# Kernel optimization log

Hardware: AMD Instinct MI355X
Metric: run time of the kernel (lower is better)

Reference implementation:

```python
import jax, jax.numpy as jnp
import numpy as np

D_MODEL = 1024
NUM_HEADS = 16
D_K = D_MODEL // NUM_HEADS
ROPE_THETA = 10000.0


def setup_inputs() -> dict:
    key = jax.random.key(0)
    kx, kq, kk, kv, ko = jax.random.split(key, 5)
    B, S = 4, 2048
    std = (2.0 / (D_MODEL + D_MODEL)) ** 0.5
    def w(k):
        return jax.random.truncated_normal(k, -3.0, 3.0, (D_MODEL, D_MODEL), jnp.float32) * std
    return {
        "x": jax.random.normal(kx, (B, S, D_MODEL), jnp.float32),
        "Wq": w(kq), "Wk": w(kk), "Wv": w(kv), "Wo": w(ko),
    }


def _apply_rope(t):
    # t: [B, H, S, d_k]
    S, dk = t.shape[-2], t.shape[-1]
    inv_freq = 1.0 / (ROPE_THETA ** (jnp.arange(0, dk, 2) / dk))  # [dk/2]
    angles = jnp.outer(jnp.arange(S), inv_freq)                    # [S, dk/2]
    cos = jnp.repeat(jnp.cos(angles), 2, axis=-1).astype(t.dtype)  # [S, dk]
    sin = jnp.repeat(jnp.sin(angles), 2, axis=-1).astype(t.dtype)
    t_even = t[..., 0::2]
    t_odd = t[..., 1::2]
    t_rot = jnp.stack([-t_odd, t_even], axis=-1).reshape(t.shape)
    return t * cos + t_rot * sin


def reference(x, Wq, Wk, Wv, Wo):
    B, S, D = x.shape
    H, dk = NUM_HEADS, D_K
    q = jnp.einsum("bsi,io->bso", x, Wq).reshape(B, S, H, dk).swapaxes(1, 2)
    k = jnp.einsum("bsi,io->bso", x, Wk).reshape(B, S, H, dk).swapaxes(1, 2)
    v = jnp.einsum("bsi,io->bso", x, Wv).reshape(B, S, H, dk).swapaxes(1, 2)
    q = _apply_rope(q)
    k = _apply_rope(k)
    scores = jnp.einsum("bhqd,bhkd->bhqk", q, k) / (dk ** 0.5)  # [B,H,S,S]
    causal = jnp.tril(jnp.ones((S, S), dtype=bool))
    scores = jnp.where(causal, scores, -jnp.inf)
    attn = jax.nn.softmax(scores, axis=-1)
    out = jnp.einsum("bhqk,bhkd->bhqd", attn, v)  # [B,H,S,dk]
    out = out.swapaxes(1, 2).reshape(B, S, D)
    return jnp.einsum("bsi,io->bso", out, Wo)
```

## Files before the change

kernel.cpp:

```cpp
#include <hip/hip_runtime.h>
#include <hip/hip_bf16.h>

#define SEQ   2048
#define NB    4
#define NH    16
#define DK    64
#define DM    1024
#define MROWS (NB * SEQ)

typedef __bf16 bf16_t;
typedef __bf16 bf16x8 __attribute__((ext_vector_type(8)));
typedef __bf16 bf16x4 __attribute__((ext_vector_type(4)));
typedef float  f32x4  __attribute__((ext_vector_type(4)));

#define MFMA16(a, b, c) __builtin_amdgcn_mfma_f32_16x16x32_bf16((a), (b), (c), 0, 0, 0)

__device__ __forceinline__ void gl2lds16(const bf16_t* g, bf16_t* l) {
    __builtin_amdgcn_global_load_lds(
        (const __attribute__((address_space(1))) unsigned int*)g,
        (__attribute__((address_space(3))) unsigned int*)l, 16, 0, 0);
}

__global__ __launch_bounds__(256) void cvt_kernel(
    const float* __restrict__ in, bf16_t* __restrict__ out, int n)
{
    int i = (blockIdx.x * 256 + threadIdx.x) * 4;
    if (i + 3 < n) {
        const float4 v = *(const float4*)(in + i);
        bf16x4 o;
        o[0] = (bf16_t)v.x; o[1] = (bf16_t)v.y;
        o[2] = (bf16_t)v.z; o[3] = (bf16_t)v.w;
        *(bf16x4*)(out + i) = o;
    }
}

__global__ __launch_bounds__(256) void wtr_kernel(
    const float* __restrict__ W, bf16_t* __restrict__ Wt)
{
    __shared__ float T[32][33];
    const int tk0 = (blockIdx.x >> 5) << 5;
    const int tn0 = (blockIdx.x & 31) << 5;
    const int r = threadIdx.x >> 5, c = threadIdx.x & 31;
#pragma unroll
    for (int i = 0; i < 4; ++i)
        T[r + i * 8][c] = W[(size_t)(tk0 + r + i * 8) * DM + tn0 + c];
    __syncthreads();
#pragma unroll
    for (int i = 0; i < 4; ++i)
        Wt[(size_t)(tn0 + r + i * 8) * DM + tk0 + c] = (bf16_t)T[c][r + i * 8];
}

__global__ void rope_table_kernel(float2* __restrict__ tab) {
    int idx = blockIdx.x * 256 + threadIdx.x;
    if (idx >= SEQ * 32) return;
    int s = idx >> 5, i = idx & 31;
    float freq = powf(10000.0f, -(float)i / 32.0f);
    float a = (float)s * freq;
    tab[idx] = make_float2(cosf(a), sinf(a));
}

#define SBAR()   asm volatile("s_barrier" ::: "memory")
#define VMC(N)   asm volatile("s_waitcnt vmcnt(" #N ")" ::: "memory")

template<bool TR>
__device__ __forceinline__ void kloop256(
    const bf16_t* __restrict__ Xp, const bf16_t* __restrict__ Wp,
    bf16_t* L, int tid, f32x4 (&acc)[8][4], int kt)
{
    const int lane = tid & 63;
    const int wave = tid >> 6;
    const int wm   = wave & 1;
    const int wn   = wave >> 1;
    const int lrow = lane & 15;
    const int lcol = (lane >> 4) << 3;

    bf16_t* const As = L;
    bf16_t* const Bs = L + 4 * 8192;

    auto stA = [&](int t, int half) {
        const bf16_t* g = Xp + (size_t)(half * 128 + wave * 16 + lrow) * DM + t * 64 + lcol;
        bf16_t* s = As + ((t & 1) * 2 + half) * 8192 + wave * 1024;
        gl2lds16(g,      s);
        gl2lds16(g + 32, s + 512);
    };
    auto stB = [&](int t, int half) {
        const bf16_t* g = Wp + (size_t)(half * 128 + wave * 16 + lrow) * DM + t * 64 + lcol;
        bf16_t* s = Bs + ((t & 1) * 2 + half) * 8192 + wave * 1024;
        gl2lds16(g,      s);
        gl2lds16(g + 32, s + 512);
    };

    const bf16_t* const Aw = As + wm * 8192;
    const bf16_t* const Bw = Bs + (wn >> 1) * 8192;
    const int bgrp = (wn & 1) * 4;

    stA(0, 0); stA(0, 1); stB(0, 0); stB(0, 1);
    stB(1, 0); stB(1, 1);
    VMC(4);
    SBAR();

    const int nit = kt >> 1;
    for (int it = 0; it < nit; ++it) {
        const int t = 2 * it;
        const bool lst = (t + 2 >= kt);

#pragma unroll
        for (int par = 0; par < 2; ++par) {
            bf16x8 bf[8];
#pragma unroll
            for (int q = 0; q < 4; ++q) {
                const bf16_t* ap = Aw + par * 16384;
                bf16x8 a00 = *(const bf16x8*)(ap + (q * 4 + 0) * 512 + lane * 8);
                bf16x8 a01 = *(const bf16x8*)(ap + (q * 4 + 1) * 512 + lane * 8);
                bf16x8 a10 = *(const bf16x8*)(ap + (q * 4 + 2) * 512 + lane * 8);
                bf16x8 a11 = *(const bf16x8*)(ap + (q * 4 + 3) * 512 + lane * 8);
                if (q == 0) {
                    const bf16_t* bp = Bw + par * 16384;
#pragma unroll
                    for (int nf = 0; nf < 4; ++nf) {
                        bf[nf * 2]     = *(const bf16x8*)(bp + ((bgrp + nf) * 2 + 0) * 512 + lane * 8);
                        bf[nf * 2 + 1] = *(const bf16x8*)(bp + ((bgrp + nf) * 2 + 1) * 512 + lane * 8);
                    }
                }
                if (par == 0) {
                    if (q == 0) { stA(t + 1, 0); stA(t + 1, 1); }
                    else if (q == 1) { if (!lst) stB(t + 2, 0); }
                    else if (q == 2) { if (!lst) stB(t + 2, 1); }
                } else {
                    if (q == 0)      { if (!lst) stA(t + 2, 0); }
                    else if (q == 1) { if (!lst) stA(t + 2, 1); }
                    else if (q == 2) { if (!lst) stB(t + 3, 0); }
                    else             { if (!lst) stB(t + 3, 1); }
                }
                SBAR();
                __builtin_amdgcn_s_setprio(1);
#pragma unroll
                for (int nf = 0; nf < 4; ++nf) {
                    if (TR) {
                        acc[q * 2 + 0][nf] = MFMA16(bf[nf * 2],     a00, acc[q * 2 + 0][nf]);
                        acc[q * 2 + 0][nf] = MFMA16(bf[nf * 2 + 1], a01, acc[q * 2 + 0][nf]);
                        acc[q * 2 + 1][nf] = MFMA16(bf[nf * 2],     a10, acc[q * 2 + 1][nf]);
                        acc[q * 2 + 1][nf] = MFMA16(bf[nf * 2 + 1], a11, acc[q * 2 + 1][nf]);
                    } else {
                        acc[q * 2 + 0][nf] = MFMA16(a00, bf[nf * 2],     acc[q * 2 + 0][nf]);
                        acc[q * 2 + 0][nf] = MFMA16(a01, bf[nf * 2 + 1], acc[q * 2 + 0][nf]);
                        acc[q * 2 + 1][nf] = MFMA16(a10, bf[nf * 2],     acc[q * 2 + 1][nf]);
                        acc[q * 2 + 1][nf] = MFMA16(a11, bf[nf * 2 + 1], acc[q * 2 + 1][nf]);
                    }
                }
                __builtin_amdgcn_s_setprio(0);
                if (q == 3) {
                    if (par == 0) { if (lst) { VMC(0); } else { VMC(4); } }
                    else          { if (!lst) { VMC(4); } }
                }
                SBAR();
            }
        }
    }
    VMC(0);
}

__global__ __launch_bounds__(512, 2) void gemm_qkv_kernel(
    const bf16_t* __restrict__ X, const bf16_t* __restrict__ Wt,
    bf16_t* __restrict__ Qt, bf16_t* __restrict__ Kt, bf16_t* __restrict__ Vtr,
    const float2* __restrict__ rope)
{
    __shared__ __align__(16) bf16_t L[8 * 8192];

    const int tid = threadIdx.x;
    const int xcd = blockIdx.x & 7;
    const int idx = blockIdx.x >> 3;
    const int mt  = xcd * 4 + idx / 12;
    const int nt  = idx % 12;
    const int m0 = mt << 8, n0 = nt << 8;
    const bool tr = (n0 >= 2 * DM);

    f32x4 acc[8][4] = {};
    if (tr) kloop256<true >(X + (size_t)m0 * DM, Wt + (size_t)n0 * DM, L, tid, acc, DM / 64);
    else    kloop256<false>(X + (size_t)m0 * DM, Wt + (size_t)n0 * DM, L, tid, acc, DM / 64);

    const int lane = tid & 63;
    const int wave = tid >> 6;
    const int wm   = wave & 1, wn = wave >> 1;
    const int l    = lane & 15;
    const int quad = lane >> 4;

#pragma unroll
    for (int mf = 0; mf < 8; ++mf)
#pragma unroll
        for (int nf = 0; nf < 4; ++nf)
#pragma unroll
            for (int r = 0; r < 4; ++r) {
                float v = acc[mf][nf][r];
                if (tr) {
                    const int n = n0 + wn * 64 + nf * 16 + quad * 4 + r;
                    const int m = m0 + wm * 128 + mf * 16 + l;
                    const int bi = m >> 11, s = m & (SEQ - 1);
                    const int col = n & (DM - 1);
                    const int h = col >> 6, d = col & (DK - 1);
                    Vtr[(((size_t)(bi * NH + h)) * DK + d) * SEQ + s] = (bf16_t)v;
                } else {
                    const int m  = m0 + wm * 128 + mf * 16 + quad * 4 + r;
                    const int nn = n0 + wn * 64 + nf * 16 + l;
                    const int bi = m >> 11, s = m & (SEQ - 1);
                    const int col = nn & (DM - 1);
                    const int h = col >> 6, d = col & (DK - 1);
                    float pv = __shfl_xor(v, 1);
                    float2 cs = rope[s * 32 + (d >> 1)];
                    float res = (d & 1) ? (v * cs.x + pv * cs.y)
                                        : (v * cs.x - pv * cs.y);
                    bf16_t* dst = (nn < DM) ? Qt : Kt;
                    if (nn < DM) res *= 0.125f;
                    dst[(((size_t)(bi * NH + h)) * SEQ + s) * DK + d] = (bf16_t)res;
                }
            }
}

__global__ __launch_bounds__(512, 2) void gemm_out_kernel(
    const bf16_t* __restrict__ X, const bf16_t* __restrict__ Wt,
    float* __restrict__ out)
{
    __shared__ __align__(16) bf16_t L[8 * 8192];

    const int tid = threadIdx.x;
    const int xcd = blockIdx.x & 7;
    const int idx = blockIdx.x >> 3;
    const int mt  = xcd * 4 + idx / 4;
    const int nt  = idx & 3;
    const int m0 = mt << 8, n0 = nt << 8;

    f32x4 acc[8][4] = {};
    kloop256<false>(X + (size_t)m0 * DM, Wt + (size_t)n0 * DM, L, tid, acc, DM / 64);

    const int lane = tid & 63;
    const int wave = tid >> 6;
    const int wm   = wave & 1, wn = wave >> 1;
    const int l    = lane & 15;
    const int quad = lane >> 4;

#pragma unroll
    for (int mf = 0; mf < 8; ++mf)
#pragma unroll
        for (int nf = 0; nf < 4; ++nf)
#pragma unroll
            for (int r = 0; r < 4; ++r) {
                const int m  = m0 + wm * 128 + mf * 16 + quad * 4 + r;
                const int nn = n0 + wn * 64 + nf * 16 + l;
                out[(size_t)m * DM + nn] = acc[mf][nf][r];
            }
}

#define KLD 72

__global__ __launch_bounds__(256) void attn_kernel(
    const bf16_t* __restrict__ Q, const bf16_t* __restrict__ K,
    const bf16_t* __restrict__ Vt, bf16_t* __restrict__ O)
{
    __shared__ __align__(16) bf16_t Kl[64 * KLD];
    __shared__ __align__(16) bf16_t Vl[64 * KLD];
    __shared__ __align__(16) bf16_t Pl[4][32 * KLD];

    const int bh   = blockIdx.x;
    const int qx   = blockIdx.y;
    const int tid  = threadIdx.x;
    const int wave = tid >> 6;
    const int lane = tid & 63;
    const int l    = lane & 15;
    const int quad = lane >> 4;
    const int srow = tid >> 3;
    const int sch  = (tid & 7) << 3;

    bf16_t* Pw = Pl[wave];
    const bf16_t* Qb = Q  + (size_t)bh * SEQ * DK;
    const bf16_t* Kb = K  + (size_t)bh * SEQ * DK;
    const bf16_t* Vb = Vt + (size_t)bh * DK * SEQ;
    const int b = bh >> 4, h = bh & 15;

    for (int ph = 0; ph < 2; ++ph) {
        const int qblk = ph ? (15 - qx) : qx;
        const int q0w  = qblk * 128 + wave * 32;
        const int nch  = 2 * (qblk + 1);

        bf16x8 qb[2][2];
#pragma unroll
        for (int u = 0; u < 2; ++u) {
            qb[u][0] = *(const bf16x8*)(Qb + (size_t)(q0w + u * 16 + l) * DK + quad * 8);
            qb[u][1] = *(const bf16x8*)(Qb + (size_t)(q0w + u * 16 + l) * DK + 32 + quad * 8);
        }

        float m_run[2] = {-3e38f, -3e38f};
        float l_run[2] = {0.f, 0.f};
        f32x4 o[4][2] = {};

        bf16x8 pk0 = *(const bf16x8*)(Kb + (size_t)srow * DK + sch);
        bf16x8 pk1 = *(const bf16x8*)(Kb + (size_t)(32 + srow) * DK + sch);
        bf16x8 pv0 = *(const bf16x8*)(Vb + (size_t)srow * SEQ + sch);
        bf16x8 pv1 = *(const bf16x8*)(Vb + (size_t)(32 + srow) * SEQ + sch);

        for (int i = 0; i < nch; ++i) {
            const int c = i * 64;
            __syncthreads();
            *(bf16x8*)(Kl + srow * KLD + sch)        = pk0;
            *(bf16x8*)(Kl + (32 + srow) * KLD + sch) = pk1;
            *(bf16x8*)(Vl + srow * KLD + sch)        = pv0;
            *(bf16x8*)(Vl + (32 + srow) * KLD + sch) = pv1;
            __syncthreads();
            if (i + 1 < nch) {
                const int cn = c + 64;
                pk0 = *(const bf16x8*)(Kb + (size_t)(cn + srow) * DK + sch);
                pk1 = *(const bf16x8*)(Kb + (size_t)(cn + 32 + srow) * DK + sch);
                pv0 = *(const bf16x8*)(Vb + (size_t)srow * SEQ + cn + sch);
                pv1 = *(const bf16x8*)(Vb + (size_t)(32 + srow) * SEQ + cn + sch);
            }
            if (c > q0w + 31) continue;

            f32x4 st[4][2] = {};
#pragma unroll
            for (int t = 0; t < 4; ++t) {
                const bf16x8 k0 = *(const bf16x8*)(Kl + (t * 16 + l) * KLD + quad * 8);
                const bf16x8 k1 = *(const bf16x8*)(Kl + (t * 16 + l) * KLD + 32 + quad * 8);
                st[t][0] = MFMA16(k0, qb[0][0], st[t][0]);
                st[t][0] = MFMA16(k1, qb[0][1], st[t][0]);
                st[t][1] = MFMA16(k0, qb[1][0], st[t][1]);
                st[t][1] = MFMA16(k1, qb[1][1], st[t][1]);
            }
            if (c + 63 > q0w) {
#pragma unroll
                for (int u = 0; u < 2; ++u) {
                    const int thr = q0w + u * 16 + l - c - quad * 4;
#pragma unroll
                    for (int t = 0; t < 4; ++t)
#pragma unroll
                        for (int r = 0; r < 4; ++r)
                            if (t * 16 + r > thr) st[t][u][r] = -3e38f;
                }
            }
#pragma unroll
            for (int u = 0; u < 2; ++u) {
                float cmax = -3e38f;
#pragma unroll
                for (int t = 0; t < 4; ++t)
#pragma unroll
                    for (int r = 0; r < 4; ++r)
                        cmax = fmaxf(cmax, st[t][u][r]);
                cmax = fmaxf(cmax, __shfl_xor(cmax, 16));
                cmax = fmaxf(cmax, __shfl_xor(cmax, 32));
                const float mnew  = fmaxf(m_run[u], cmax);
                const float alpha = __expf(m_run[u] - mnew);
                m_run[u] = mnew;
                float csum = 0.f;
#pragma unroll
                for (int t = 0; t < 4; ++t)
#pragma unroll
                    for (int r = 0; r < 4; ++r) {
                        st[t][u][r] = __expf(st[t][u][r] - mnew);
                        csum += st[t][u][r];
                    }
                csum += __shfl_xor(csum, 16);
                csum += __shfl_xor(csum, 32);
                l_run[u] = l_run[u] * alpha + csum;
#pragma unroll
                for (int n = 0; n < 4; ++n)
#pragma unroll
                    for (int r = 0; r < 4; ++r)
                        o[n][u][r] *= alpha;
#pragma unroll
                for (int t = 0; t < 4; ++t) {
                    bf16x4 pk;
                    pk[0] = (bf16_t)st[t][u][0]; pk[1] = (bf16_t)st[t][u][1];
                    pk[2] = (bf16_t)st[t][u][2]; pk[3] = (bf16_t)st[t][u][3];
                    *(bf16x4*)(Pw + (u * 16 + l) * KLD + t * 16 + quad * 4) = pk;
                }
            }
            const bf16x8 pb00 = *(const bf16x8*)(Pw + l * KLD + quad * 8);
            const bf16x8 pb01 = *(const bf16x8*)(Pw + l * KLD + 32 + quad * 8);
            const bf16x8 pb10 = *(const bf16x8*)(Pw + (16 + l) * KLD + quad * 8);
            const bf16x8 pb11 = *(const bf16x8*)(Pw + (16 + l) * KLD + 32 + quad * 8);
#pragma unroll
            for (int n = 0; n < 4; ++n) {
                const bf16x8 v0 = *(const bf16x8*)(Vl + (n * 16 + l) * KLD + quad * 8);
                const bf16x8 v1 = *(const bf16x8*)(Vl + (n * 16 + l) * KLD + 32 + quad * 8);
                o[n][0] = MFMA16(v0, pb00, o[n][0]);
                o[n][0] = MFMA16(v1, pb01, o[n][0]);
                o[n][1] = MFMA16(v0, pb10, o[n][1]);
                o[n][1] = MFMA16(v1, pb11, o[n][1]);
            }
        }

#pragma unroll
        for (int u = 0; u < 2; ++u) {
            const float inv = 1.0f / l_run[u];
#pragma unroll
            for (int n = 0; n < 4; ++n) {
                bf16x4 ov;
                ov[0] = (bf16_t)(o[n][u][0] * inv); ov[1] = (bf16_t)(o[n][u][1] * inv);
                ov[2] = (bf16_t)(o[n][u][2] * inv); ov[3] = (bf16_t)(o[n][u][3] * inv);
                *(bf16x4*)(Pw + (u * 16 + l) * KLD + n * 16 + quad * 4) = ov;
            }
        }
        const int row  = lane >> 1;
        const int half = (lane & 1) * 32;
        const bf16x8 w0 = *(const bf16x8*)(Pw + row * KLD + half);
        const bf16x8 w1 = *(const bf16x8*)(Pw + row * KLD + half + 8);
        const bf16x8 w2 = *(const bf16x8*)(Pw + row * KLD + half + 16);
        const bf16x8 w3 = *(const bf16x8*)(Pw + row * KLD + half + 24);
        bf16_t* op = O + ((size_t)(b * SEQ + qblk * 128 + wave * 32 + row)) * DM
                       + h * DK + half;
        *(bf16x8*)(op)      = w0;
        *(bf16x8*)(op + 8)  = w1;
        *(bf16x8*)(op + 16) = w2;
        *(bf16x8*)(op + 24) = w3;
    }
}

extern "C" void kernel_launch(void* const* d_in, const int* in_sizes, int n_in,
                              void* d_out, int out_size, void* d_ws, size_t ws_size,
                              hipStream_t stream)
{
    const float* x  = (const float*)d_in[0];
    const float* Wq = (const float*)d_in[1];
    const float* Wk = (const float*)d_in[2];
    const float* Wv = (const float*)d_in[3];
    const float* Wo = (const float*)d_in[4];

    char* ws = (char*)d_ws;
    float2* rope = (float2*)ws;
    const size_t TEN = (size_t)MROWS * DM;
    const size_t WEL = (size_t)DM * DM;
    bf16_t* xb    = (bf16_t*)(ws + (1 << 19));
    bf16_t* Wqkvt = xb + TEN;
    bf16_t* Wot   = Wqkvt + 3 * WEL;
    bf16_t* Qt    = Wot + WEL;
    bf16_t* Kt    = Qt + TEN;
    bf16_t* Vt    = Kt + TEN;
    bf16_t* Ot    = Vt + TEN;

    rope_table_kernel<<<(SEQ * 32 + 255) / 256, 256, 0, stream>>>(rope);

    cvt_kernel<<<(int)(TEN / 4 / 256), 256, 0, stream>>>(x, xb, (int)TEN);
    wtr_kernel<<<1024, 256, 0, stream>>>(Wq, Wqkvt);
    wtr_kernel<<<1024, 256, 0, stream>>>(Wk, Wqkvt + WEL);
    wtr_kernel<<<1024, 256, 0, stream>>>(Wv, Wqkvt + 2 * WEL);
    wtr_kernel<<<1024, 256, 0, stream>>>(Wo, Wot);

    gemm_qkv_kernel<<<32 * 12, 512, 0, stream>>>(xb, Wqkvt, Qt, Kt, Vt, rope);

    attn_kernel<<<dim3(NB * NH, 8), 256, 0, stream>>>(Qt, Kt, Vt, Ot);

    gemm_out_kernel<<<32 * 4, 512, 0, stream>>>(Ot, Wot, (float*)d_out);
}
```

Before: 328.2 us.

## Halve GEMM M-tile to 128 and restructure the k-loop pipeline for more blocks

The QKV and output projection GEMMs drop from 256x256 to 128x256 tiles. This doubles the grid (768 and 256 blocks) so work spreads better across the GPU's CUs, and it shrinks LDS to 96KB per block. The k-loop is rewritten with a new LDS staging layout and explicit four-phase prefetch of A and B sub-tiles, and the per-XCD block mapping is updated to match. The trade-off is lower arithmetic intensity per tile, since more B traffic is needed per FLOP.

```diff
diff --git a/kernel.cpp b/kernel.cpp
--- a/kernel.cpp
+++ b/kernel.cpp
@@ -20,6 +20,9 @@
         (const __attribute__((address_space(1))) unsigned int*)g,
         (__attribute__((address_space(3))) unsigned int*)l, 16, 0, 0);
 }
+
+#define SBAR()   asm volatile("s_barrier" ::: "memory")
+#define VMC(N)   asm volatile("s_waitcnt vmcnt(" #N ")" ::: "memory")
 
 __global__ __launch_bounds__(256) void cvt_kernel(
     const float* __restrict__ in, bf16_t* __restrict__ out, int n)
@@ -59,105 +62,136 @@
     tab[idx] = make_float2(cosf(a), sinf(a));
 }
 
-#define SBAR()   asm volatile("s_barrier" ::: "memory")
-#define VMC(N)   asm volatile("s_waitcnt vmcnt(" #N ")" ::: "memory")
-
 template<bool TR>
-__device__ __forceinline__ void kloop256(
+__device__ __forceinline__ void kloop(
     const bf16_t* __restrict__ Xp, const bf16_t* __restrict__ Wp,
-    bf16_t* L, int tid, f32x4 (&acc)[8][4], int kt)
+    bf16_t* L, int tid, f32x4 (&acc)[4][4])
 {
     const int lane = tid & 63;
     const int wave = tid >> 6;
     const int wm   = wave & 1;
     const int wn   = wave >> 1;
+    const int bh   = wn >> 1;
+    const int bg   = wn & 1;
     const int lrow = lane & 15;
     const int lcol = (lane >> 4) << 3;
 
     bf16_t* const As = L;
-    bf16_t* const Bs = L + 4 * 8192;
-
-    auto stA = [&](int t, int half) {
-        const bf16_t* g = Xp + (size_t)(half * 128 + wave * 16 + lrow) * DM + t * 64 + lcol;
-        bf16_t* s = As + ((t & 1) * 2 + half) * 8192 + wave * 1024;
-        gl2lds16(g,      s);
-        gl2lds16(g + 32, s + 512);
-    };
-    auto stB = [&](int t, int half) {
-        const bf16_t* g = Wp + (size_t)(half * 128 + wave * 16 + lrow) * DM + t * 64 + lcol;
-        bf16_t* s = Bs + ((t & 1) * 2 + half) * 8192 + wave * 1024;
-        gl2lds16(g,      s);
-        gl2lds16(g + 32, s + 512);
-    };
-
-    const bf16_t* const Aw = As + wm * 8192;
-    const bf16_t* const Bw = Bs + (wn >> 1) * 8192;
-    const int bgrp = (wn & 1) * 4;
-
-    stA(0, 0); stA(0, 1); stB(0, 0); stB(0, 1);
-    stB(1, 0); stB(1, 1);
+    bf16_t* const Bs = L + 16384;
+
+    const bf16_t* pA0 = Xp + (size_t)(wn * 16 + lrow) * DM + wm * 32 + lcol;
+    const bf16_t* pA1 = pA0 + (size_t)64 * DM;
+    const bf16_t* pB0 = Wp + (size_t)(wave * 16 + lrow) * DM + lcol;
+    const bf16_t* pB1 = pB0 + (size_t)128 * DM;
+
+    bf16_t* const aldsw = As + wave * 512;
+    bf16_t* const bldsw = Bs + wave * 1024;
+
+    const bf16_t* const Ard = As + wm * 4096;
+    const bf16_t* const Brd = Bs + bh * 8192 + bg * 4096;
+
+    gl2lds16(pA0,      aldsw);
+    gl2lds16(pA1,      aldsw + 4096);
+    gl2lds16(pB0,      bldsw);
+    gl2lds16(pB0 + 32, bldsw + 512);
+    gl2lds16(pB1,      bldsw + 8192);
+    gl2lds16(pB1 + 32, bldsw + 8704);
+    gl2lds16(pB0 + 64, bldsw + 16384);
+    gl2lds16(pB0 + 96, bldsw + 16896);
+    gl2lds16(pB1 + 64, bldsw + 24576);
+    gl2lds16(pB1 + 96, bldsw + 25088);
     VMC(4);
     SBAR();
 
-    const int nit = kt >> 1;
+#define PHASE_MMA(MF0, A0, A1, A2, A3)                                       \
+    __builtin_amdgcn_s_setprio(1);                                           \
+    _Pragma("unroll")                                                        \
+    for (int nf = 0; nf < 4; ++nf) {                                         \
+        if (TR) {                                                            \
+            acc[MF0][nf]     = MFMA16(bf[nf*2],   A0, acc[MF0][nf]);         \
+            acc[MF0][nf]     = MFMA16(bf[nf*2+1], A1, acc[MF0][nf]);         \
+            acc[MF0+1][nf]   = MFMA16(bf[nf*2],   A2, acc[MF0+1][nf]);       \
+            acc[MF0+1][nf]   = MFMA16(bf[nf*2+1], A3, acc[MF0+1][nf]);       \
+        } else {                                                             \
+            acc[MF0][nf]     = MFMA16(A0, bf[nf*2],   acc[MF0][nf]);         \
+            acc[MF0][nf]     = MFMA16(A1, bf[nf*2+1], acc[MF0][nf]);         \
+            acc[MF0+1][nf]   = MFMA16(A2, bf[nf*2],   acc[MF0+1][nf]);       \
+            acc[MF0+1][nf]   = MFMA16(A3, bf[nf*2+1], acc[MF0+1][nf]);       \
+        }                                                                    \
+    }                                                                        \
+    __builtin_amdgcn_s_setprio(0);
+
+    const int nit = (DM / 64) >> 1;
     for (int it = 0; it < nit; ++it) {
-        const int t = 2 * it;
-        const bool lst = (t + 2 >= kt);
-
-#pragma unroll
-        for (int par = 0; par < 2; ++par) {
-            bf16x8 bf[8];
-#pragma unroll
-            for (int q = 0; q < 4; ++q) {
-                const bf16_t* ap = Aw + par * 16384;
-                bf16x8 a00 = *(const bf16x8*)(ap + (q * 4 + 0) * 512 + lane * 8);
-                bf16x8 a01 = *(const bf16x8*)(ap + (q * 4 + 1) * 512 + lane * 8);
-                bf16x8 a10 = *(const bf16x8*)(ap + (q * 4 + 2) * 512 + lane * 8);
-                bf16x8 a11 = *(const bf16x8*)(ap + (q * 4 + 3) * 512 + lane * 8);
-                if (q == 0) {
-                    const bf16_t* bp = Bw + par * 16384;
-#pragma unroll
-                    for (int nf = 0; nf < 4; ++nf) {
-                        bf[nf * 2]     = *(const bf16x8*)(bp + ((bgrp + nf) * 2 + 0) * 512 + lane * 8);
-                        bf[nf * 2 + 1] = *(const bf16x8*)(bp + ((bgrp + nf) * 2 + 1) * 512 + lane * 8);
-                    }
-                }
-                if (par == 0) {
-                    if (q == 0) { stA(t + 1, 0); stA(t + 1, 1); }
-                    else if (q == 1) { if (!lst) stB(t + 2, 0); }
-                    else if (q == 2) { if (!lst) stB(t + 2, 1); }
-                } else {
-                    if (q == 0)      { if (!lst) stA(t + 2, 0); }
-                    else if (q == 1) { if (!lst) stA(t + 2, 1); }
-                    else if (q == 2) { if (!lst) stB(t + 3, 0); }
-                    else             { if (!lst) stB(t + 3, 1); }
-                }
-                SBAR();
-                __builtin_amdgcn_s_setprio(1);
-#pragma unroll
-                for (int nf = 0; nf < 4; ++nf) {
-                    if (TR) {
-                        acc[q * 2 + 0][nf] = MFMA16(bf[nf * 2],     a00, acc[q * 2 + 0][nf]);
-                        acc[q * 2 + 0][nf] = MFMA16(bf[nf * 2 + 1], a01, acc[q * 2 + 0][nf]);
-                        acc[q * 2 + 1][nf] = MFMA16(bf[nf * 2],     a10, acc[q * 2 + 1][nf]);
-                        acc[q * 2 + 1][nf] = MFMA16(bf[nf * 2 + 1], a11, acc[q * 2 + 1][nf]);
-                    } else {
-                        acc[q * 2 + 0][nf] = MFMA16(a00, bf[nf * 2],     acc[q * 2 + 0][nf]);
-                        acc[q * 2 + 0][nf] = MFMA16(a01, bf[nf * 2 + 1], acc[q * 2 + 0][nf]);
-                        acc[q * 2 + 1][nf] = MFMA16(a10, bf[nf * 2],     acc[q * 2 + 1][nf]);
-                        acc[q * 2 + 1][nf] = MFMA16(a11, bf[nf * 2 + 1], acc[q * 2 + 1][nf]);
-                    }
-                }
-                __builtin_amdgcn_s_setprio(0);
-                if (q == 3) {
-                    if (par == 0) { if (lst) { VMC(0); } else { VMC(4); } }
-                    else          { if (!lst) { VMC(4); } }
-                }
-                SBAR();
-            }
-        }
+        const bool lst = (it == nit - 1);
+        bf16x8 bf[8];
+        bf16x8 a0, a1, a2, a3;
+
+#pragma unroll
+        for (int nf = 0; nf < 4; ++nf) {
+            bf[nf * 2]     = *(const bf16x8*)(Brd + nf * 1024 + lane * 8);
+            bf[nf * 2 + 1] = *(const bf16x8*)(Brd + nf * 1024 + 512 + lane * 8);
+        }
+        a0 = *(const bf16x8*)(Ard + 0 * 512 + lane * 8);
+        a1 = *(const bf16x8*)(Ard + 1 * 512 + lane * 8);
+        a2 = *(const bf16x8*)(Ard + 2 * 512 + lane * 8);
+        a3 = *(const bf16x8*)(Ard + 3 * 512 + lane * 8);
+        gl2lds16(pA0 + 64, aldsw + 8192);
+        gl2lds16(pA1 + 64, aldsw + 12288);
+        SBAR();
+        PHASE_MMA(0, a0, a1, a2, a3)
+        SBAR();
+
+        a0 = *(const bf16x8*)(Ard + 4 * 512 + lane * 8);
+        a1 = *(const bf16x8*)(Ard + 5 * 512 + lane * 8);
+        a2 = *(const bf16x8*)(Ard + 6 * 512 + lane * 8);
+        a3 = *(const bf16x8*)(Ard + 7 * 512 + lane * 8);
+        if (!lst) {
+            gl2lds16(pB0 + 128, bldsw);
+            gl2lds16(pB0 + 160, bldsw + 512);
+            gl2lds16(pB1 + 128, bldsw + 8192);
+            gl2lds16(pB1 + 160, bldsw + 8704);
+        }
+        SBAR();
+        PHASE_MMA(2, a0, a1, a2, a3)
+        if (lst) { VMC(0); } else { VMC(4); }
+        SBAR();
+
+#pragma unroll
+        for (int nf = 0; nf < 4; ++nf) {
+            bf[nf * 2]     = *(const bf16x8*)(Brd + 16384 + nf * 1024 + lane * 8);
+            bf[nf * 2 + 1] = *(const bf16x8*)(Brd + 16384 + nf * 1024 + 512 + lane * 8);
+        }
+        a0 = *(const bf16x8*)(Ard + 8192 + 0 * 512 + lane * 8);
+        a1 = *(const bf16x8*)(Ard + 8192 + 1 * 512 + lane * 8);
+        a2 = *(const bf16x8*)(Ard + 8192 + 2 * 512 + lane * 8);
+        a3 = *(const bf16x8*)(Ard + 8192 + 3 * 512 + lane * 8);
+        if (!lst) {
+            gl2lds16(pA0 + 128, aldsw);
+            gl2lds16(pA1 + 128, aldsw + 4096);
+        }
+        SBAR();
+        PHASE_MMA(0, a0, a1, a2, a3)
+        SBAR();
+
+        a0 = *(const bf16x8*)(Ard + 8192 + 4 * 512 + lane * 8);
+        a1 = *(const bf16x8*)(Ard + 8192 + 5 * 512 + lane * 8);
+        a2 = *(const bf16x8*)(Ard + 8192 + 6 * 512 + lane * 8);
+        a3 = *(const bf16x8*)(Ard + 8192 + 7 * 512 + lane * 8);
+        if (!lst) {
+            gl2lds16(pB0 + 192, bldsw + 16384);
+            gl2lds16(pB0 + 224, bldsw + 16896);
+            gl2lds16(pB1 + 192, bldsw + 24576);
+            gl2lds16(pB1 + 224, bldsw + 25088);
+        }
+        SBAR();
+        PHASE_MMA(2, a0, a1, a2, a3)
+        if (lst) { VMC(0); } else { VMC(4); }
+        SBAR();
+
+        pA0 += 128; pA1 += 128; pB0 += 128; pB1 += 128;
     }
-    VMC(0);
+#undef PHASE_MMA
 }
 
 __global__ __launch_bounds__(512, 2) void gemm_qkv_kernel(
@@ -165,19 +199,19 @@
     bf16_t* __restrict__ Qt, bf16_t* __restrict__ Kt, bf16_t* __restrict__ Vtr,
     const float2* __restrict__ rope)
 {
-    __shared__ __align__(16) bf16_t L[8 * 8192];
+    __shared__ __align__(16) bf16_t L[49152];
 
     const int tid = threadIdx.x;
     const int xcd = blockIdx.x & 7;
     const int idx = blockIdx.x >> 3;
-    const int mt  = xcd * 4 + idx / 12;
-    const int nt  = idx % 12;
-    const int m0 = mt << 8, n0 = nt << 8;
+    const int mt  = xcd * 8 + (idx & 7);
+    const int nt  = idx >> 3;
+    const int m0 = mt << 7, n0 = nt << 8;
     const bool tr = (n0 >= 2 * DM);
 
-    f32x4 acc[8][4] = {};
-    if (tr) kloop256<true >(X + (size_t)m0 * DM, Wt + (size_t)n0 * DM, L, tid, acc, DM / 64);
-    else    kloop256<false>(X + (size_t)m0 * DM, Wt + (size_t)n0 * DM, L, tid, acc, DM / 64);
+    f32x4 acc[4][4] = {};
+    if (tr) kloop<true >(X + (size_t)m0 * DM, Wt + (size_t)n0 * DM, L, tid, acc);
+    else    kloop<false>(X + (size_t)m0 * DM, Wt + (size_t)n0 * DM, L, tid, acc);
 
     const int lane = tid & 63;
     const int wave = tid >> 6;
@@ -186,7 +220,7 @@
     const int quad = lane >> 4;
 
 #pragma unroll
-    for (int mf = 0; mf < 8; ++mf)
+    for (int mf = 0; mf < 4; ++mf)
 #pragma unroll
         for (int nf = 0; nf < 4; ++nf)
 #pragma unroll
@@ -194,13 +228,13 @@
                 float v = acc[mf][nf][r];
                 if (tr) {
                     const int n = n0 + wn * 64 + nf * 16 + quad * 4 + r;
-                    const int m = m0 + wm * 128 + mf * 16 + l;
+                    const int m = m0 + wm * 64 + mf * 16 + l;
                     const int bi = m >> 11, s = m & (SEQ - 1);
                     const int col = n & (DM - 1);
                     const int h = col >> 6, d = col & (DK - 1);
                     Vtr[(((size_t)(bi * NH + h)) * DK + d) * SEQ + s] = (bf16_t)v;
                 } else {
-                    const int m  = m0 + wm * 128 + mf * 16 + quad * 4 + r;
+                    const int m  = m0 + wm * 64 + mf * 16 + quad * 4 + r;
                     const int nn = n0 + wn * 64 + nf * 16 + l;
                     const int bi = m >> 11, s = m & (SEQ - 1);
                     const int col = nn & (DM - 1);
@@ -220,17 +254,17 @@
     const bf16_t* __restrict__ X, const bf16_t* __restrict__ Wt,
     float* __restrict__ out)
 {
-    __shared__ __align__(16) bf16_t L[8 * 8192];
+    __shared__ __align__(16) bf16_t L[49152];
 
     const int tid = threadIdx.x;
     const int xcd = blockIdx.x & 7;
     const int idx = blockIdx.x >> 3;
-    const int mt  = xcd * 4 + idx / 4;
-    const int nt  = idx & 3;
-    const int m0 = mt << 8, n0 = nt << 8;
-
-    f32x4 acc[8][4] = {};
-    kloop256<false>(X + (size_t)m0 * DM, Wt + (size_t)n0 * DM, L, tid, acc, DM / 64);
+    const int mt  = xcd * 8 + (idx & 7);
+    const int nt  = idx >> 3;
+    const int m0 = mt << 7, n0 = nt << 8;
+
+    f32x4 acc[4][4] = {};
+    kloop<false>(X + (size_t)m0 * DM, Wt + (size_t)n0 * DM, L, tid, acc);
 
     const int lane = tid & 63;
     const int wave = tid >> 6;
@@ -239,12 +273,12 @@
     const int quad = lane >> 4;
 
 #pragma unroll
-    for (int mf = 0; mf < 8; ++mf)
+    for (int mf = 0; mf < 4; ++mf)
 #pragma unroll
         for (int nf = 0; nf < 4; ++nf)
 #pragma unroll
             for (int r = 0; r < 4; ++r) {
-                const int m  = m0 + wm * 128 + mf * 16 + quad * 4 + r;
+                const int m  = m0 + wm * 64 + mf * 16 + quad * 4 + r;
                 const int nn = n0 + wn * 64 + nf * 16 + l;
                 out[(size_t)m * DM + nn] = acc[mf][nf][r];
             }
@@ -443,9 +477,9 @@
     wtr_kernel<<<1024, 256, 0, stream>>>(Wv, Wqkvt + 2 * WEL);
     wtr_kernel<<<1024, 256, 0, stream>>>(Wo, Wot);
 
-    gemm_qkv_kernel<<<32 * 12, 512, 0, stream>>>(xb, Wqkvt, Qt, Kt, Vt, rope);
+    gemm_qkv_kernel<<<64 * 12, 512, 0, stream>>>(xb, Wqkvt, Qt, Kt, Vt, rope);
 
     attn_kernel<<<dim3(NB * NH, 8), 256, 0, stream>>>(Qt, Kt, Vt, Ot);
 
-    gemm_out_kernel<<<32 * 4, 512, 0, stream>>>(Ot, Wot, (float*)d_out);
-}
+    gemm_out_kernel<<<64 * 4, 512, 0, stream>>>(Ot, Wot, (float*)d_out);
+}
```

Result: faster. 308.5 us (-6.0%).

## Rewrite GEMM k-loop with register double-buffered LDS fragments and new wave mapping

Applied to the files above, without the earlier changes.

Replaces the GEMM main loop with a fully unrolled, macro-driven schedule. LDS fragment reads for the next quarter-step are prefetched into registers (double-buffered A and B fragments) while the current MFMAs run, and global-to-LDS loads are interleaved at finer granularity with adjusted waitcnts. The wave-to-tile mapping changes so each wave owns a 64-column B slice, and block-to-tile ordering is swapped to group N tiles per XCD. The goal is to hide LDS read latency behind MFMA work, at the cost of higher register pressure and a hard-coded K of 1024.

```diff
diff --git a/kernel.cpp b/kernel.cpp
--- a/kernel.cpp
+++ b/kernel.cpp
@@ -20,6 +20,9 @@
         (const __attribute__((address_space(1))) unsigned int*)g,
         (__attribute__((address_space(3))) unsigned int*)l, 16, 0, 0);
 }
+
+#define SBAR()   asm volatile("s_barrier" ::: "memory")
+#define VMC(N)   asm volatile("s_waitcnt vmcnt(" #N ")" ::: "memory")
 
 __global__ __launch_bounds__(256) void cvt_kernel(
     const float* __restrict__ in, bf16_t* __restrict__ out, int n)
@@ -59,105 +62,135 @@
     tab[idx] = make_float2(cosf(a), sinf(a));
 }
 
-#define SBAR()   asm volatile("s_barrier" ::: "memory")
-#define VMC(N)   asm volatile("s_waitcnt vmcnt(" #N ")" ::: "memory")
-
 template<bool TR>
-__device__ __forceinline__ void kloop256(
+__device__ __forceinline__ void kloop(
     const bf16_t* __restrict__ Xp, const bf16_t* __restrict__ Wp,
-    bf16_t* L, int tid, f32x4 (&acc)[8][4], int kt)
+    bf16_t* L, int tid, f32x4 (&acc)[8][4])
 {
     const int lane = tid & 63;
     const int wave = tid >> 6;
-    const int wm   = wave & 1;
-    const int wn   = wave >> 1;
+    const int wm   = wave >> 2;
+    const int wn   = wave & 3;
     const int lrow = lane & 15;
     const int lcol = (lane >> 4) << 3;
 
-    bf16_t* const As = L;
-    bf16_t* const Bs = L + 4 * 8192;
-
-    auto stA = [&](int t, int half) {
-        const bf16_t* g = Xp + (size_t)(half * 128 + wave * 16 + lrow) * DM + t * 64 + lcol;
-        bf16_t* s = As + ((t & 1) * 2 + half) * 8192 + wave * 1024;
-        gl2lds16(g,      s);
-        gl2lds16(g + 32, s + 512);
-    };
-    auto stB = [&](int t, int half) {
-        const bf16_t* g = Wp + (size_t)(half * 128 + wave * 16 + lrow) * DM + t * 64 + lcol;
-        bf16_t* s = Bs + ((t & 1) * 2 + half) * 8192 + wave * 1024;
-        gl2lds16(g,      s);
-        gl2lds16(g + 32, s + 512);
-    };
-
-    const bf16_t* const Aw = As + wm * 8192;
-    const bf16_t* const Bw = Bs + (wn >> 1) * 8192;
-    const int bgrp = (wn & 1) * 4;
-
-    stA(0, 0); stA(0, 1); stB(0, 0); stB(0, 1);
-    stB(1, 0); stB(1, 1);
-    VMC(4);
+    bf16_t* const AR = L;
+    bf16_t* const BR = L + 32768;
+
+    const bf16_t* pA0 = Xp + (size_t)(wave * 16 + lrow) * DM + lcol;
+    const bf16_t* pA1 = pA0 + (size_t)128 * DM;
+    const bf16_t* pB0 = Wp + (size_t)(wave * 16 + lrow) * DM + lcol;
+    const bf16_t* pB1 = pB0 + (size_t)128 * DM;
+
+    bf16_t* const adst = AR + wave * 1024;
+    bf16_t* const bdst = BR + wave * 1024;
+
+    const bf16_t* const Ard = AR + wm * 8192;
+    const bf16_t* const Brd = BR + wn * 4096;
+
+    bf16x8 a0[2][2], a1[2][2], bc[4][2], bn[4][2];
+
+#define RD_A(BUF, Q, D)                                                       \
+    D[0][0] = *(const bf16x8*)(Ard + (BUF) + (2*(Q)+0)*1024 + lane*8);        \
+    D[0][1] = *(const bf16x8*)(Ard + (BUF) + (2*(Q)+0)*1024 + 512 + lane*8);  \
+    D[1][0] = *(const bf16x8*)(Ard + (BUF) + (2*(Q)+1)*1024 + lane*8);        \
+    D[1][1] = *(const bf16x8*)(Ard + (BUF) + (2*(Q)+1)*1024 + 512 + lane*8);
+
+#define RD_B(BUF, NF, D)                                                      \
+    D[NF][0] = *(const bf16x8*)(Brd + (BUF) + (NF)*1024 + lane*8);            \
+    D[NF][1] = *(const bf16x8*)(Brd + (BUF) + (NF)*1024 + 512 + lane*8);
+
+#define ST_A(BUF, H, C)                                                       \
+    gl2lds16(((H) ? pA1 : pA0) + (C),      adst + (BUF) + (H)*8192);          \
+    gl2lds16(((H) ? pA1 : pA0) + (C) + 32, adst + (BUF) + (H)*8192 + 512);
+
+#define ST_B(BUF, H, C)                                                       \
+    gl2lds16(((H) ? pB1 : pB0) + (C),      bdst + (BUF) + (H)*8192);          \
+    gl2lds16(((H) ? pB1 : pB0) + (C) + 32, bdst + (BUF) + (H)*8192 + 512);
+
+#define QMMA(Q, A, B)                                                         \
+    __builtin_amdgcn_s_setprio(1);                                            \
+    _Pragma("unroll")                                                         \
+    for (int nf = 0; nf < 4; ++nf) {                                          \
+        if (TR) {                                                             \
+            acc[2*(Q)][nf]   = MFMA16(B[nf][0], A[0][0], acc[2*(Q)][nf]);     \
+            acc[2*(Q)][nf]   = MFMA16(B[nf][1], A[0][1], acc[2*(Q)][nf]);     \
+            acc[2*(Q)+1][nf] = MFMA16(B[nf][0], A[1][0], acc[2*(Q)+1][nf]);   \
+            acc[2*(Q)+1][nf] = MFMA16(B[nf][1], A[1][1], acc[2*(Q)+1][nf]);   \
+        } else {                                                              \
+            acc[2*(Q)][nf]   = MFMA16(A[0][0], B[nf][0], acc[2*(Q)][nf]);     \
+            acc[2*(Q)][nf]   = MFMA16(A[0][1], B[nf][1], acc[2*(Q)][nf]);     \
+            acc[2*(Q)+1][nf] = MFMA16(A[1][0], B[nf][0], acc[2*(Q)+1][nf]);   \
+            acc[2*(Q)+1][nf] = MFMA16(A[1][1], B[nf][1], acc[2*(Q)+1][nf]);   \
+        }                                                                     \
+    }                                                                         \
+    __builtin_amdgcn_s_setprio(0);
+
+#define ITER(LST)                                                             \
+                                                              \
+    VMC(4); SBAR();                                                           \
+    RD_A(0, 1, a1) RD_B(16384, 0, bn)                                         \
+    if (!(LST)) { ST_B(0, 0, 128) }                                           \
+    QMMA(0, a0, bc)                                                           \
+                                                              \
+    SBAR();                                                                   \
+    RD_A(0, 2, a0) RD_B(16384, 1, bn)                                         \
+    if (!(LST)) { ST_B(0, 1, 128) }                                           \
+    QMMA(1, a1, bc)                                                           \
+                                                              \
+    SBAR();                                                                   \
+    RD_A(0, 3, a1) RD_B(16384, 2, bn)                                         \
+    QMMA(2, a0, bc)                                                           \
+                                                              \
+    if (LST) { VMC(0); } else { VMC(4); }                                     \
+    SBAR();                                                                   \
+    RD_A(16384, 0, a0) RD_B(16384, 3, bn)                                     \
+    if (!(LST)) { ST_A(0, 0, 128) }                                           \
+    QMMA(3, a1, bc)                                                           \
+                                                            \
+    if (!(LST)) { VMC(2); }                                                   \
+    SBAR();                                                                   \
+    RD_A(16384, 1, a1) RD_B(0, 0, bc)                                         \
+    if (!(LST)) { ST_A(0, 1, 128) }                                           \
+    QMMA(0, a0, bn)                                                           \
+                                                            \
+    SBAR();                                                                   \
+    RD_A(16384, 2, a0) RD_B(0, 1, bc)                                         \
+    if (!(LST)) { ST_B(16384, 0, 192) }                                       \
+    QMMA(1, a1, bn)                                                           \
+                                                            \
+    SBAR();                                                                   \
+    RD_A(16384, 3, a1) RD_B(0, 2, bc)                                         \
+    if (!(LST)) { ST_B(16384, 1, 192) }                                       \
+    QMMA(2, a0, bn)                                                           \
+                                                            \
+    if (!(LST)) { VMC(4); }                                                   \
+    SBAR();                                                                   \
+    RD_A(0, 0, a0) RD_B(0, 3, bc)                                             \
+    if (!(LST)) { ST_A(16384, 0, 192) ST_A(16384, 1, 192) }                   \
+    QMMA(3, a1, bn)
+
+    ST_A(0, 0, 0) ST_A(0, 1, 0)
+    ST_B(0, 0, 0) ST_B(0, 1, 0)
+    ST_B(16384, 0, 64) ST_B(16384, 1, 64)
+    ST_A(16384, 0, 64) ST_A(16384, 1, 64)
+    VMC(8);
     SBAR();
-
-    const int nit = kt >> 1;
-    for (int it = 0; it < nit; ++it) {
-        const int t = 2 * it;
-        const bool lst = (t + 2 >= kt);
-
-#pragma unroll
-        for (int par = 0; par < 2; ++par) {
-            bf16x8 bf[8];
-#pragma unroll
-            for (int q = 0; q < 4; ++q) {
-                const bf16_t* ap = Aw + par * 16384;
-                bf16x8 a00 = *(const bf16x8*)(ap + (q * 4 + 0) * 512 + lane * 8);
-                bf16x8 a01 = *(const bf16x8*)(ap + (q * 4 + 1) * 512 + lane * 8);
-                bf16x8 a10 = *(const bf16x8*)(ap + (q * 4 + 2) * 512 + lane * 8);
-                bf16x8 a11 = *(const bf16x8*)(ap + (q * 4 + 3) * 512 + lane * 8);
-                if (q == 0) {
-                    const bf16_t* bp = Bw + par * 16384;
-#pragma unroll
-                    for (int nf = 0; nf < 4; ++nf) {
-                        bf[nf * 2]     = *(const bf16x8*)(bp + ((bgrp + nf) * 2 + 0) * 512 + lane * 8);
-                        bf[nf * 2 + 1] = *(const bf16x8*)(bp + ((bgrp + nf) * 2 + 1) * 512 + lane * 8);
-                    }
-                }
-                if (par == 0) {
-                    if (q == 0) { stA(t + 1, 0); stA(t + 1, 1); }
-                    else if (q == 1) { if (!lst) stB(t + 2, 0); }
-                    else if (q == 2) { if (!lst) stB(t + 2, 1); }
-                } else {
-                    if (q == 0)      { if (!lst) stA(t + 2, 0); }
-                    else if (q == 1) { if (!lst) stA(t + 2, 1); }
-                    else if (q == 2) { if (!lst) stB(t + 3, 0); }
-                    else             { if (!lst) stB(t + 3, 1); }
-                }
-                SBAR();
-                __builtin_amdgcn_s_setprio(1);
-#pragma unroll
-                for (int nf = 0; nf < 4; ++nf) {
-                    if (TR) {
-                        acc[q * 2 + 0][nf] = MFMA16(bf[nf * 2],     a00, acc[q * 2 + 0][nf]);
-                        acc[q * 2 + 0][nf] = MFMA16(bf[nf * 2 + 1], a01, acc[q * 2 + 0][nf]);
-                        acc[q * 2 + 1][nf] = MFMA16(bf[nf * 2],     a10, acc[q * 2 + 1][nf]);
-                        acc[q * 2 + 1][nf] = MFMA16(bf[nf * 2 + 1], a11, acc[q * 2 + 1][nf]);
-                    } else {
-                        acc[q * 2 + 0][nf] = MFMA16(a00, bf[nf * 2],     acc[q * 2 + 0][nf]);
-                        acc[q * 2 + 0][nf] = MFMA16(a01, bf[nf * 2 + 1], acc[q * 2 + 0][nf]);
-                        acc[q * 2 + 1][nf] = MFMA16(a10, bf[nf * 2],     acc[q * 2 + 1][nf]);
-                        acc[q * 2 + 1][nf] = MFMA16(a11, bf[nf * 2 + 1], acc[q * 2 + 1][nf]);
-                    }
-                }
-                __builtin_amdgcn_s_setprio(0);
-                if (q == 3) {
-                    if (par == 0) { if (lst) { VMC(0); } else { VMC(4); } }
-                    else          { if (!lst) { VMC(4); } }
-                }
-                SBAR();
-            }
-        }
+    RD_A(0, 0, a0)
+    RD_B(0, 0, bc) RD_B(0, 1, bc) RD_B(0, 2, bc) RD_B(0, 3, bc)
+
+    for (int it = 0; it < 7; ++it) {
+        ITER(0)
+        pA0 += 128; pA1 += 128; pB0 += 128; pB1 += 128;
     }
-    VMC(0);
+    ITER(1)
+
+#undef ITER
+#undef QMMA
+#undef ST_B
+#undef ST_A
+#undef RD_B
+#undef RD_A
 }
 
 __global__ __launch_bounds__(512, 2) void gemm_qkv_kernel(
@@ -165,23 +198,23 @@
     bf16_t* __restrict__ Qt, bf16_t* __restrict__ Kt, bf16_t* __restrict__ Vtr,
     const float2* __restrict__ rope)
 {
-    __shared__ __align__(16) bf16_t L[8 * 8192];
+    __shared__ __align__(16) bf16_t L[65536];
 
     const int tid = threadIdx.x;
     const int xcd = blockIdx.x & 7;
     const int idx = blockIdx.x >> 3;
-    const int mt  = xcd * 4 + idx / 12;
-    const int nt  = idx % 12;
+    const int mt  = xcd * 4 + (idx & 3);
+    const int nt  = idx >> 2;
     const int m0 = mt << 8, n0 = nt << 8;
     const bool tr = (n0 >= 2 * DM);
 
     f32x4 acc[8][4] = {};
-    if (tr) kloop256<true >(X + (size_t)m0 * DM, Wt + (size_t)n0 * DM, L, tid, acc, DM / 64);
-    else    kloop256<false>(X + (size_t)m0 * DM, Wt + (size_t)n0 * DM, L, tid, acc, DM / 64);
+    if (tr) kloop<true >(X + (size_t)m0 * DM, Wt + (size_t)n0 * DM, L, tid, acc);
+    else    kloop<false>(X + (size_t)m0 * DM, Wt + (size_t)n0 * DM, L, tid, acc);
 
     const int lane = tid & 63;
     const int wave = tid >> 6;
-    const int wm   = wave & 1, wn = wave >> 1;
+    const int wm   = wave >> 2, wn = wave & 3;
     const int l    = lane & 15;
     const int quad = lane >> 4;
 
@@ -220,21 +253,21 @@
     const bf16_t* __restrict__ X, const bf16_t* __restrict__ Wt,
     float* __restrict__ out)
 {
-    __shared__ __align__(16) bf16_t L[8 * 8192];
+    __shared__ __align__(16) bf16_t L[65536];
 
     const int tid = threadIdx.x;
     const int xcd = blockIdx.x & 7;
     const int idx = blockIdx.x >> 3;
-    const int mt  = xcd * 4 + idx / 4;
-    const int nt  = idx & 3;
+    const int mt  = xcd * 4 + (idx & 3);
+    const int nt  = idx >> 2;
     const int m0 = mt << 8, n0 = nt << 8;
 
     f32x4 acc[8][4] = {};
-    kloop256<false>(X + (size_t)m0 * DM, Wt + (size_t)n0 * DM, L, tid, acc, DM / 64);
+    kloop<false>(X + (size_t)m0 * DM, Wt + (size_t)n0 * DM, L, tid, acc);
 
     const int lane = tid & 63;
     const int wave = tid >> 6;
-    const int wm   = wave & 1, wn = wave >> 1;
+    const int wm   = wave >> 2, wn = wave & 3;
     const int l    = lane & 15;
     const int quad = lane >> 4;
 
```

Measured after the change: 313.1 us. 4.6% less time.
